# Kernel tuning notes

Hardware: AMD Instinct MI355X
Metric: run time of the kernel (lower is better)

Reference implementation:

```python
import jax, jax.numpy as jnp
import numpy as np

D_MODEL = 1024
N_HEAD = 16
D_QKV = 64
INIT_RANGE = 0.02
BOUND = float(np.sqrt(3.0) * INIT_RANGE)
SCALE = 1.0 / D_QKV ** 0.5


def setup_inputs() -> dict:
    key = jax.random.key(0)
    kx, k1, k2, k3, k4 = jax.random.split(key, 5)
    B, T = 4, 2048
    x = jax.random.normal(kx, (B, T, D_MODEL), dtype=jnp.float32)
    half_f = D_MODEL // 2
    half_a = D_QKV // 2
    u = lambda k, shp: jax.random.uniform(k, shp, dtype=jnp.float32, minval=-BOUND, maxval=BOUND)
    w_qkv_c = u(k1, (N_HEAD, half_f, 3, half_a))
    w_qkv_p = u(k2, (N_HEAD, half_f, 3, half_a))
    w_o_c = u(k3, (N_HEAD, half_a, half_f))
    w_o_p = u(k4, (N_HEAD, half_a, half_f))
    return {"x": x, "w_qkv_c": w_qkv_c, "w_qkv_p": w_qkv_p, "w_o_c": w_o_c, "w_o_p": w_o_p}


def reference(x, w_qkv_c, w_qkv_p, w_o_c, w_o_p):
    x_c, x_p = jnp.split(x, 2, axis=-1)  # [B,T,d_model//2] each
    # partitioned QKV projections: [B,H,T,3,a/2]
    qkv_c = jnp.einsum('btf,hfca->bhtca', x_c, w_qkv_c)
    qkv_p = jnp.einsum('btf,hfca->bhtca', x_p, w_qkv_p)
    q_c, k_c, v_c = qkv_c[:, :, :, 0], qkv_c[:, :, :, 1], qkv_c[:, :, :, 2]
    q_p, k_p, v_p = qkv_p[:, :, :, 0], qkv_p[:, :, :, 1], qkv_p[:, :, :, 2]
    q = jnp.concatenate([q_c, q_p], axis=-1) * SCALE  # [B,H,T,d_qkv]
    k = jnp.concatenate([k_c, k_p], axis=-1)
    v = jnp.concatenate([v_c, v_p], axis=-1)
    dots = jnp.einsum('bhqa,bhka->bhqk', q, k)  # [B,H,T,T]
    probs = jax.nn.softmax(dots, axis=-1)
    o = jnp.einsum('bhqk,bhka->bhqa', probs, v)  # [B,H,T,d_qkv]
    o_c, o_p = jnp.split(o, 2, axis=-1)
    out_c = jnp.einsum('bhta,haf->btf', o_c, w_o_c)
    out_p = jnp.einsum('bhta,haf->btf', o_p, w_o_p)
    return (out_c, out_p)
```

## Files before the change

### kernel.cpp

```cpp
#include <hip/hip_runtime.h>


typedef __attribute__((ext_vector_type(8))) short bf16x8;
typedef __attribute__((ext_vector_type(4))) float f32x4;
typedef unsigned short u16;

#define QSCALE 0.18033688011112042f

__device__ __forceinline__ u16 f2bf(float f){
  unsigned u = __builtin_bit_cast(unsigned, f);
  u += 0x7FFFu + ((u >> 16) & 1u);
  return (u16)(u >> 16);
}

__device__ __forceinline__ unsigned cvtpk(float lo, float hi){
  unsigned r;
  asm("v_cvt_pk_bf16_f32 %0, %1, %2" : "=v"(r) : "v"(lo), "v"(hi));
  return r;
}

__device__ __forceinline__ float fexp2(float s){
  float fi = __builtin_rintf(s);
  float f  = s - fi;
  float p  = __builtin_fmaf(f, __builtin_fmaf(f, 0.2426039f, 0.6951588f), 0.9999365f);
  return __builtin_amdgcn_ldexpf(p, (int)fi);
}

__global__ __launch_bounds__(256) void k_prep(const float4* __restrict__ x, u16* __restrict__ xA,
                                              const float* __restrict__ wqc, const float* __restrict__ wqp,
                                              u16* __restrict__ wqt,
                                              const float* __restrict__ woc, const float* __restrict__ wop,
                                              u16* __restrict__ wot){
  const unsigned blk = blockIdx.x;
  if (blk < 8192u){
    unsigned i = blk*256 + threadIdx.x;
    float4 v = x[i];
    unsigned j = i*4;
    unsigned row = j >> 10, col = j & 1023u;
    unsigned tile = row >> 4, li = row & 15u;
    unsigned part = col >> 9, ks = (col >> 5) & 15u, lg = (col >> 3) & 3u, e = col & 7u;
    uint2 pk;
    pk.x = (unsigned)f2bf(v.x) | ((unsigned)f2bf(v.y) << 16);
    pk.y = (unsigned)f2bf(v.z) | ((unsigned)f2bf(v.w) << 16);
    *(uint2*)(xA + (size_t)(((tile*2 + part)*16 + ks)*512) + li*32 + lg*8 + e) = pk;
  } else if (blk < 14336u){
    unsigned i = (blk - 8192u)*256 + threadIdx.x;
    unsigned ph = i / 49152u;
    unsigned r  = i - ph*49152u;
    unsigned ks = r / 3072u;
    unsigned r2 = r - ks*3072u;
    unsigned n  = r2 >> 9;
    unsigned r3 = r2 & 511u;
    unsigned lg = r3 >> 7, li = (r3 >> 3) & 15u, e = r3 & 7u;
    unsigned h = ph & 15u;
    unsigned f = ks*32u + lg*8u + e;
    const float* src = (ph < 16) ? wqc : wqp;
    wqt[i] = f2bf(src[h*49152u + f*96u + (n>>1)*32u + (n&1u)*16u + li]);
  } else {
    unsigned i = (blk - 14336u)*256 + threadIdx.x;
    unsigned e = i & 7u;
    unsigned lane = (i >> 3) & 63u;
    unsigned n  = (i >> 9) & 7u;
    unsigned ks = (i >> 12) & 15u;
    unsigned ft = (i >> 16) & 3u;
    unsigned part = i >> 18;
    unsigned f = ft*128u + n*16u + (lane & 15u);
    unsigned a = (lane >> 4)*8u + e;
    const float* src = part ? wop : woc;
    wot[i] = f2bf(src[ks*16384u + a*512u + f]);
  }
}

__global__ __launch_bounds__(256) void k_qkv(const u16* __restrict__ xA, const u16* __restrict__ wt,
                                             u16* __restrict__ Q, u16* __restrict__ K, u16* __restrict__ VT){
  const int lane = threadIdx.x & 63, wv = threadIdx.x >> 6;
  const int lg = lane >> 4, li = lane & 15;
  const int blk = blockIdx.x;
  const int xcd = blk & 7, idx = blk >> 3;
  const int tt  = (idx >> 5)*8 + xcd;
  const int ph  = idx & 31;
  const int row0 = tt*256 + wv*64;
  const int part = ph >> 4, h = ph & 15;

  f32x4 acc[4][6] = {};
  const u16* wbase = wt + (size_t)ph*49152;
  const unsigned aoff = (unsigned)(li*32 + lg*8);
  #pragma unroll 2
  for (int ks = 0; ks < 16; ++ks){
    bf16x8 a[4], b[6];
    #pragma unroll
    for (int m=0;m<4;++m)
      a[m] = *(const bf16x8*)(xA + (size_t)(((tt*16 + wv*4 + m)*2 + part)*16 + ks)*512 + aoff);
    #pragma unroll
    for (int n=0;n<6;++n)
      b[n] = *(const bf16x8*)(wbase + ks*3072 + n*512 + lane*8);
    #pragma unroll
    for (int m=0;m<4;++m)
      #pragma unroll
      for (int n=0;n<6;++n)
        acc[m][n] = __builtin_amdgcn_mfma_f32_16x16x32_bf16(a[m], b[n], acc[m][n], 0, 0, 0);
  }

  const int b_ = row0 >> 11;
  const int bh = b_*16 + h;
  const int tl0 = (row0 & 2047) + lg*4;
  #pragma unroll
  for (int m=0;m<4;++m){
    #pragma unroll
    for (int n=0;n<6;++n){
      const int c = n >> 1;
      const int af = part*32 + (n & 1)*16 + li;
      if (c == 2){
        uint2 pk;
        pk.x = (unsigned)f2bf(acc[m][n][0]) | ((unsigned)f2bf(acc[m][n][1]) << 16);
        pk.y = (unsigned)f2bf(acc[m][n][2]) | ((unsigned)f2bf(acc[m][n][3]) << 16);
        const int kt = ((row0 & 2047) >> 5) + (m>>1);
        u16* dst = VT + (size_t)bh*131072 + (size_t)kt*2048
                 + (part*2 + (n&1))*512 + ((m&1)*2 + (lg>>1))*128 + li*8 + (lg&1)*4;
        *(uint2*)dst = pk;
      } else if (c == 1){
        const unsigned kb = ((unsigned)(af>>5))*512 + ((unsigned)((af>>3)&3))*128 + (unsigned)(af&7);
        #pragma unroll
        for (int r=0;r<4;++r){
          int t = tl0 + m*16 + r;
          K[(size_t)bh*131072 + (t>>5)*2048 + ((t>>4)&1)*1024 + kb + (t&15)*8] = f2bf(acc[m][n][r]);
        }
      } else {
        #pragma unroll
        for (int r=0;r<4;++r){
          int t = tl0 + m*16 + r;
          Q[((size_t)bh*2048 + t)*64 + af] = f2bf(acc[m][n][r] * QSCALE);
        }
      }
    }
  }
}

#define NKT 64
#define PLD 40
__global__ __launch_bounds__(256, 4) void k_attn(const u16* __restrict__ Q, const u16* __restrict__ K,
                                                 const u16* __restrict__ VT, u16* __restrict__ OA){
  __shared__ __align__(16) char smem[20480];
  const int lane = threadIdx.x & 63, w = threadIdx.x >> 6;
  const int lg = lane >> 4, li = lane & 15;
  const int swz = (blockIdx.x & 7)*128 + (blockIdx.x >> 3);
  const int bh = swz >> 4, qt = swz & 15;
  const int q0 = qt*128 + w*32;

  const char* Kfb = (const char*)K + (size_t)bh*262144;
  const char* Vfb = (const char*)VT + (size_t)bh*262144;
  const u16*  Qb  = Q + (size_t)bh*131072;
  u16* pw = (u16*)smem + w*2560;

  bf16x8 aq[2][2];
  #pragma unroll
  for (int m=0;m<2;++m)
    #pragma unroll
    for (int kd=0;kd<2;++kd)
      aq[m][kd] = *(const bf16x8*)(Qb + (size_t)(q0 + m*16 + li)*64 + kd*32 + lg*8);

  const short one_bf = (short)0x3F80;
  bf16x8 ones = {one_bf,one_bf,one_bf,one_bf,one_bf,one_bf,one_bf,one_bf};

  f32x4 o[2][4] = {};
  f32x4 ls[2] = {};
  bf16x8 ka0_00, ka0_01, ka0_10, ka0_11;
  bf16x8 ka1_00, ka1_01, ka1_10, ka1_11;
  bf16x8 va_0, va_1, va_2, va_3;

#define KLOAD(BANK, KT) { const char* kb_ = Kfb + (size_t)(KT)*4096; \
    ka##BANK##_00 = *(const bf16x8*)(kb_ +        lane*16); \
    ka##BANK##_01 = *(const bf16x8*)(kb_ + 1024 + lane*16); \
    ka##BANK##_10 = *(const bf16x8*)(kb_ + 2048 + lane*16); \
    ka##BANK##_11 = *(const bf16x8*)(kb_ + 3072 + lane*16); }
#define VLOAD(KT) { const char* vb_ = Vfb + (size_t)(KT)*4096; \
    va_0 = *(const bf16x8*)(vb_ +        lane*16); \
    va_1 = *(const bf16x8*)(vb_ + 1024 + lane*16); \
    va_2 = *(const bf16x8*)(vb_ + 2048 + lane*16); \
    va_3 = *(const bf16x8*)(vb_ + 3072 + lane*16); }

  auto QKEXP = [&](bf16x8 b00, bf16x8 b01, bf16x8 b10, bf16x8 b11, u16* pW){
    #pragma unroll
    for (int n=0;n<2;++n){
      bf16x8 bk0 = n ? b10 : b00;
      bf16x8 bk1 = n ? b11 : b01;
      #pragma unroll
      for (int m=0;m<2;++m){
        f32x4 s = {0.f,0.f,0.f,0.f};
        s = __builtin_amdgcn_mfma_f32_16x16x32_bf16(bk0, aq[m][0], s, 0, 0, 0);
        s = __builtin_amdgcn_mfma_f32_16x16x32_bf16(bk1, aq[m][1], s, 0, 0, 0);
        uint2 pk;
        pk.x = cvtpk(fexp2(s[0]), fexp2(s[1]));
        pk.y = cvtpk(fexp2(s[2]), fexp2(s[3]));
        *(uint2*)(pW + (size_t)(m*16 + li)*PLD + n*16 + lg*4) = pk;
      }
    }
  };
  auto PV = [&](const u16* pR){
    bf16x8 pa0 = *(const bf16x8*)(pR + (size_t)(     li)*PLD + lg*8);
    bf16x8 pa1 = *(const bf16x8*)(pR + (size_t)(16 + li)*PLD + lg*8);
    __builtin_amdgcn_s_setprio(1);
    o[0][0] = __builtin_amdgcn_mfma_f32_16x16x32_bf16(pa0, va_0, o[0][0], 0, 0, 0);
    o[1][0] = __builtin_amdgcn_mfma_f32_16x16x32_bf16(pa1, va_0, o[1][0], 0, 0, 0);
    o[0][1] = __builtin_amdgcn_mfma_f32_16x16x32_bf16(pa0, va_1, o[0][1], 0, 0, 0);
    o[1][1] = __builtin_amdgcn_mfma_f32_16x16x32_bf16(pa1, va_1, o[1][1], 0, 0, 0);
    o[0][2] = __builtin_amdgcn_mfma_f32_16x16x32_bf16(pa0, va_2, o[0][2], 0, 0, 0);
    o[1][2] = __builtin_amdgcn_mfma_f32_16x16x32_bf16(pa1, va_2, o[1][2], 0, 0, 0);
    o[0][3] = __builtin_amdgcn_mfma_f32_16x16x32_bf16(pa0, va_3, o[0][3], 0, 0, 0);
    o[1][3] = __builtin_amdgcn_mfma_f32_16x16x32_bf16(pa1, va_3, o[1][3], 0, 0, 0);
    ls[0] = __builtin_amdgcn_mfma_f32_16x16x32_bf16(pa0, ones, ls[0], 0, 0, 0);
    ls[1] = __builtin_amdgcn_mfma_f32_16x16x32_bf16(pa1, ones, ls[1], 0, 0, 0);
    __builtin_amdgcn_s_setprio(0);
  };

#define AITER(KT, PR, PN) { \
    if ((KT) + 2 < NKT) KLOAD(PR, (KT)+2); \
    QKEXP(ka##PN##_00, ka##PN##_01, ka##PN##_10, ka##PN##_11, pw + (PN)*1280); \
    PV(pw + (PR)*1280); \
    if ((KT) + 1 < NKT) VLOAD((KT)+1); }

  KLOAD(0, 0);
  KLOAD(1, 1);
  VLOAD(0);
  QKEXP(ka0_00, ka0_01, ka0_10, ka0_11, pw);

  for (int base = 0; base < NKT-2; base += 2){
    AITER(base,   0, 1);
    AITER(base+1, 1, 0);
  }
  AITER(NKT-2, 0, 1);
  PV(pw + 1280);

  const int b_ = bh >> 4, h = bh & 15;
  #pragma unroll
  for (int m=0;m<2;++m){
    const int tile = (b_*2048 + q0 + m*16) >> 4;
    #pragma unroll
    for (int r=0;r<4;++r){
      float linv = 1.0f / ls[m][r];
      #pragma unroll
      for (int nd=0;nd<4;++nd){
        OA[(size_t)(((tile*16 + h)*2 + (nd>>1))*512)
           + (lg*4 + r)*32 + ((nd&1)*2 + (li>>3))*8 + (li&7)] = f2bf(o[m][nd][r] * linv);
      }
    }
  }
#undef AITER
#undef KLOAD
#undef VLOAD
}

__global__ __launch_bounds__(256) void k_proj(const u16* __restrict__ OA, const u16* __restrict__ wot,
                                              float* __restrict__ out){
  const int lane = threadIdx.x & 63, wv = threadIdx.x >> 6;
  const int lg = lane >> 4, li = lane & 15;
  const int blk = blockIdx.x;
  const int xcd = blk & 7, idx = blk >> 3;
  const int rowTile = (idx >> 3)*8 + xcd;
  const int colTile = idx & 7;
  const int row0 = rowTile*128 + wv*32;
  const int part = colTile >> 2;
  const int ft   = colTile & 3;
  const int f0   = ft*128;

  f32x4 acc[2][8] = {};
  const u16* wbase = wot + (size_t)part*262144 + (size_t)ft*65536;
  const unsigned aoff = (unsigned)(li*32 + lg*8);
  #pragma unroll 4
  for (int ks = 0; ks < 16; ++ks){
    bf16x8 a[2];
    #pragma unroll
    for (int m=0;m<2;++m)
      a[m] = *(const bf16x8*)(OA + (size_t)((((rowTile*8 + wv*2 + m)*16 + ks)*2 + part)*512) + aoff);
    #pragma unroll
    for (int n=0;n<8;++n){
      bf16x8 b = *(const bf16x8*)(wbase + ks*4096 + n*512 + lane*8);
      #pragma unroll
      for (int m=0;m<2;++m)
        acc[m][n] = __builtin_amdgcn_mfma_f32_16x16x32_bf16(a[m], b, acc[m][n], 0, 0, 0);
    }
  }
  float* obp = out + (size_t)part*(8192u*512u);
  #pragma unroll
  for (int m=0;m<2;++m)
    #pragma unroll
    for (int n=0;n<8;++n)
      #pragma unroll
      for (int r=0;r<4;++r)
        obp[(size_t)(row0 + m*16 + lg*4 + r)*512 + f0 + n*16 + li] = acc[m][n][r];
}

extern "C" void kernel_launch(void* const* d_in, const int* in_sizes, int n_in,
                              void* d_out, int out_size, void* d_ws, size_t ws_size,
                              hipStream_t stream){
  const float* x   = (const float*)d_in[0];
  const float* wqc = (const float*)d_in[1];
  const float* wqp = (const float*)d_in[2];
  const float* woc = (const float*)d_in[3];
  const float* wop = (const float*)d_in[4];

  char* ws = (char*)d_ws;
  u16* xA  = (u16*)(ws);
  u16* Q   = (u16*)(ws + 16777216);
  u16* K   = (u16*)(ws + 2*16777216);
  u16* VT  = (u16*)(ws + 3*16777216);
  u16* wqt = (u16*)(ws + 4*16777216);
  u16* wot = (u16*)(ws + 4*16777216 + 3145728);
  u16* OA  = xA;
  float* out = (float*)d_out;

  k_prep <<<16384, 256, 0, stream>>>((const float4*)x, xA, wqc, wqp, wqt, woc, wop, wot);
  k_qkv  <<<1024,  256, 0, stream>>>(xA, wqt, Q, K, VT);
  k_attn <<<1024,  256, 0, stream>>>(Q, K, VT, OA);
  k_proj <<<512,   256, 0, stream>>>(OA, wot, out);
}
```

Baseline: 167.5 us.

## Stage GEMM weights through LDS via async loads and vectorize weight prep

The weight-transpose paths in k_prep now have each thread produce 8 bf16 values with packed conversion and a 16-byte store, which cuts that part of the grid from about 8192 blocks to about 1024. In k_qkv and k_proj, weight tiles are loaded into double-buffered LDS with global_load_lds, so each tile is fetched once per block and shared across the four waves instead of each wave loading it from global memory. This adds a __syncthreads per k-step and some LDS footprint, and the barriers may limit overlap between loads and MFMA.

Result: faster. 153.1 us, median of 2 (-8.6%).

```diff
diff --git a/kernel.cpp b/kernel.cpp
--- a/kernel.cpp
+++ b/kernel.cpp
@@ -24,6 +24,12 @@
   float f  = s - fi;
   float p  = __builtin_fmaf(f, __builtin_fmaf(f, 0.2426039f, 0.6951588f), 0.9999365f);
   return __builtin_amdgcn_ldexpf(p, (int)fi);
+}
+
+__device__ __forceinline__ void gload16(const void* g, void* l){
+  __builtin_amdgcn_global_load_lds(
+    (const __attribute__((address_space(1))) unsigned*)g,
+    (__attribute__((address_space(3))) unsigned*)l, 16, 0, 0);
 }
 
 __global__ __launch_bounds__(256) void k_prep(const float4* __restrict__ x, u16* __restrict__ xA,
@@ -43,37 +49,45 @@
     pk.x = (unsigned)f2bf(v.x) | ((unsigned)f2bf(v.y) << 16);
     pk.y = (unsigned)f2bf(v.z) | ((unsigned)f2bf(v.w) << 16);
     *(uint2*)(xA + (size_t)(((tile*2 + part)*16 + ks)*512) + li*32 + lg*8 + e) = pk;
-  } else if (blk < 14336u){
+  } else if (blk < 8960u){
     unsigned i = (blk - 8192u)*256 + threadIdx.x;
-    unsigned ph = i / 49152u;
-    unsigned r  = i - ph*49152u;
-    unsigned ks = r / 3072u;
-    unsigned r2 = r - ks*3072u;
-    unsigned n  = r2 >> 9;
-    unsigned r3 = r2 & 511u;
-    unsigned lg = r3 >> 7, li = (r3 >> 3) & 15u, e = r3 & 7u;
+    unsigned lane = i & 63u;
+    unsigned n  = (i >> 6) % 6u;
+    unsigned ks = (i / 384u) & 15u;
+    unsigned ph = i / 6144u;
+    unsigned lg = lane >> 4, li = lane & 15u;
     unsigned h = ph & 15u;
-    unsigned f = ks*32u + lg*8u + e;
     const float* src = (ph < 16) ? wqc : wqp;
-    wqt[i] = f2bf(src[h*49152u + f*96u + (n>>1)*32u + (n&1u)*16u + li]);
+    const float* sp = src + h*49152u + (ks*32u + lg*8u)*96u + (n>>1)*32u + (n&1u)*16u + li;
+    float v0 = sp[0*96], v1 = sp[1*96], v2 = sp[2*96], v3 = sp[3*96];
+    float v4 = sp[4*96], v5 = sp[5*96], v6 = sp[6*96], v7 = sp[7*96];
+    uint4 o;
+    o.x = cvtpk(v0, v1); o.y = cvtpk(v2, v3); o.z = cvtpk(v4, v5); o.w = cvtpk(v6, v7);
+    *(uint4*)(wqt + (size_t)i*8) = o;
   } else {
-    unsigned i = (blk - 14336u)*256 + threadIdx.x;
-    unsigned e = i & 7u;
-    unsigned lane = (i >> 3) & 63u;
-    unsigned n  = (i >> 9) & 7u;
-    unsigned ks = (i >> 12) & 15u;
-    unsigned ft = (i >> 16) & 3u;
-    unsigned part = i >> 18;
+    unsigned i = (blk - 8960u)*256 + threadIdx.x;
+    unsigned lane = i & 63u;
+    unsigned n  = (i >> 6) & 7u;
+    unsigned ks = (i >> 9) & 15u;
+    unsigned ft = (i >> 13) & 3u;
+    unsigned part = i >> 15;
     unsigned f = ft*128u + n*16u + (lane & 15u);
-    unsigned a = (lane >> 4)*8u + e;
+    unsigned a0 = (lane >> 4)*8u;
     const float* src = part ? wop : woc;
-    wot[i] = f2bf(src[ks*16384u + a*512u + f]);
+    const float* sp = src + ks*16384u + a0*512u + f;
+    float v0 = sp[0*512], v1 = sp[1*512], v2 = sp[2*512], v3 = sp[3*512];
+    float v4 = sp[4*512], v5 = sp[5*512], v6 = sp[6*512], v7 = sp[7*512];
+    uint4 o;
+    o.x = cvtpk(v0, v1); o.y = cvtpk(v2, v3); o.z = cvtpk(v4, v5); o.w = cvtpk(v6, v7);
+    *(uint4*)(wot + (size_t)i*8) = o;
   }
 }
 
 __global__ __launch_bounds__(256) void k_qkv(const u16* __restrict__ xA, const u16* __restrict__ wt,
                                              u16* __restrict__ Q, u16* __restrict__ K, u16* __restrict__ VT){
+  __shared__ __align__(16) char sw[24576];
   const int lane = threadIdx.x & 63, wv = threadIdx.x >> 6;
+  const int tid = threadIdx.x;
   const int lg = lane >> 4, li = lane & 15;
   const int blk = blockIdx.x;
   const int xcd = blk & 7, idx = blk >> 3;
@@ -83,23 +97,38 @@
   const int part = ph >> 4, h = ph & 15;
 
   f32x4 acc[4][6] = {};
-  const u16* wbase = wt + (size_t)ph*49152;
+  const char* wg = (const char*)(wt + (size_t)ph*49152);
   const unsigned aoff = (unsigned)(li*32 + lg*8);
-  #pragma unroll 2
-  for (int ks = 0; ks < 16; ++ks){
-    bf16x8 a[4], b[6];
-    #pragma unroll
-    for (int m=0;m<4;++m)
-      a[m] = *(const bf16x8*)(xA + (size_t)(((tt*16 + wv*4 + m)*2 + part)*16 + ks)*512 + aoff);
-    #pragma unroll
-    for (int n=0;n<6;++n)
-      b[n] = *(const bf16x8*)(wbase + ks*3072 + n*512 + lane*8);
-    #pragma unroll
-    for (int m=0;m<4;++m)
+
+#define WSTAGE(KS2, BUF) { \
+    gload16(wg + (KS2)*12288 +        tid*16, sw + (BUF)*12288 +        wv*1024); \
+    gload16(wg + (KS2)*12288 + 4096 + tid*16, sw + (BUF)*12288 + 4096 + wv*1024); \
+    gload16(wg + (KS2)*12288 + 8192 + tid*16, sw + (BUF)*12288 + 8192 + wv*1024); }
+
+  WSTAGE(0, 0);
+  __syncthreads();
+  for (int ks2 = 0; ks2 < 8; ++ks2){
+    if (ks2 < 7) WSTAGE(ks2+1, (ks2+1)&1);
+    const char* swc = sw + (ks2&1)*12288;
+    #pragma unroll
+    for (int t = 0; t < 2; ++t){
+      const int ks = ks2*2 + t;
+      bf16x8 a[4], b[6];
+      #pragma unroll
+      for (int m=0;m<4;++m)
+        a[m] = *(const bf16x8*)(xA + (size_t)(((tt*16 + wv*4 + m)*2 + part)*16 + ks)*512 + aoff);
       #pragma unroll
       for (int n=0;n<6;++n)
-        acc[m][n] = __builtin_amdgcn_mfma_f32_16x16x32_bf16(a[m], b[n], acc[m][n], 0, 0, 0);
-  }
+        b[n] = *(const bf16x8*)(swc + t*6144 + n*1024 + lane*16);
+      #pragma unroll
+      for (int m=0;m<4;++m)
+        #pragma unroll
+        for (int n=0;n<6;++n)
+          acc[m][n] = __builtin_amdgcn_mfma_f32_16x16x32_bf16(a[m], b[n], acc[m][n], 0, 0, 0);
+    }
+    __syncthreads();
+  }
+#undef WSTAGE
 
   const int b_ = row0 >> 11;
   const int bh = b_*16 + h;
@@ -252,7 +281,9 @@
 
 __global__ __launch_bounds__(256) void k_proj(const u16* __restrict__ OA, const u16* __restrict__ wot,
                                               float* __restrict__ out){
+  __shared__ __align__(16) char swp[16384];
   const int lane = threadIdx.x & 63, wv = threadIdx.x >> 6;
+  const int tid = threadIdx.x;
   const int lg = lane >> 4, li = lane & 15;
   const int blk = blockIdx.x;
   const int xcd = blk & 7, idx = blk >> 3;
@@ -264,22 +295,33 @@
   const int f0   = ft*128;
 
   f32x4 acc[2][8] = {};
-  const u16* wbase = wot + (size_t)part*262144 + (size_t)ft*65536;
+  const char* wg = (const char*)(wot + (size_t)part*262144 + (size_t)ft*65536);
   const unsigned aoff = (unsigned)(li*32 + lg*8);
-  #pragma unroll 4
+
+#define WSTAGE(KS, BUF) { \
+    gload16(wg + (KS)*8192 +        tid*16, swp + (BUF)*8192 +        wv*1024); \
+    gload16(wg + (KS)*8192 + 4096 + tid*16, swp + (BUF)*8192 + 4096 + wv*1024); }
+
+  WSTAGE(0, 0);
+  __syncthreads();
   for (int ks = 0; ks < 16; ++ks){
+    if (ks < 15) WSTAGE(ks+1, (ks+1)&1);
+    const char* swc = swp + (ks&1)*8192;
     bf16x8 a[2];
     #pragma unroll
     for (int m=0;m<2;++m)
       a[m] = *(const bf16x8*)(OA + (size_t)((((rowTile*8 + wv*2 + m)*16 + ks)*2 + part)*512) + aoff);
     #pragma unroll
     for (int n=0;n<8;++n){
-      bf16x8 b = *(const bf16x8*)(wbase + ks*4096 + n*512 + lane*8);
+      bf16x8 b = *(const bf16x8*)(swc + n*1024 + lane*16);
       #pragma unroll
       for (int m=0;m<2;++m)
         acc[m][n] = __builtin_amdgcn_mfma_f32_16x16x32_bf16(a[m], b, acc[m][n], 0, 0, 0);
     }
-  }
+    __syncthreads();
+  }
+#undef WSTAGE
+
   float* obp = out + (size_t)part*(8192u*512u);
   #pragma unroll
   for (int m=0;m<2;++m)
@@ -309,7 +351,7 @@
   u16* OA  = xA;
   float* out = (float*)d_out;
 
-  k_prep <<<16384, 256, 0, stream>>>((const float4*)x, xA, wqc, wqp, wqt, woc, wop, wot);
+  k_prep <<<9216,  256, 0, stream>>>((const float4*)x, xA, wqc, wqp, wqt, woc, wop, wot);
   k_qkv  <<<1024,  256, 0, stream>>>(xA, wqt, Q, K, VT);
   k_attn <<<1024,  256, 0, stream>>>(Q, K, VT, OA);
   k_proj <<<512,   256, 0, stream>>>(OA, wot, out);
```
